# Performance work log

Measured on AMD Instinct MI355X. Metric: run time of the kernel, lower is better.

The kernel has to match this reference:

```python
import jax, jax.numpy as jnp
import numpy as np

# Dims: B batch, C=P channels (features per pixel), H*W=N pixels, M ELM models, Q=1 hidden units
M, Q, B, C, H, W_SP = 4, 1, 32, 1024, 28, 28
P = C
N = H * W_SP
EPS = 1e-10


def _lcg_weights(m, n, seed):
    """Deterministic LCG pseudo-random weights, z-score standardized (ELM_AE init)."""
    L = m * n
    a, b, c = L + 2, L + 3, float(L) ** 2
    v = np.zeros(L, dtype=np.float64)
    v[0] = seed + 1.0
    for i in range(1, L):
        v[i] = (a * v[i - 1] + b) % c
    v = (v - v.mean()) / (v.std() + EPS)
    return v.reshape(m, n).astype(np.float32)


def setup_inputs() -> dict:
    key = jax.random.key(0)
    x = jax.random.normal(key, (B, C, H, W_SP), dtype=jnp.float32)
    # One Q x P random input-weight matrix per ELM model, seed = model * (Q * P)
    Wm = jnp.stack([jnp.asarray(_lcg_weights(Q, P, model * (Q * P))) for model in range(M)])  # [M, Q, P]
    return {"x": x, "Wm": Wm}


def reference(x, Wm):
    b, c, h, w = x.shape
    # _norm('l2', ...): per-channel L2 normalization over (h, w), as F.normalize(dim=(1,2))
    norms = jnp.linalg.norm(x.reshape(b, c, h * w), axis=-1)[:, :, None, None]  # [B, C, 1, 1]
    xn = x / jnp.maximum(norms, EPS)
    X = xn.reshape(b, c, h * w)  # meta activation map per sample: [B, P, N]
    # ELM-AE hidden layer, batched over (sample, model): g = sigmoid(W @ X)
    G = jax.nn.sigmoid(jnp.einsum('mqp,bpn->bmqn', Wm, X))  # [B, M, Q, N]
    # fit_AE: output weights beta = pinv(g^T) @ X^T  -> [Q, P]
    pinvGt = jnp.linalg.pinv(jnp.swapaxes(G, -1, -2))       # [B, M, Q, N]
    beta = jnp.einsum('bmqn,bpn->bmqp', pinvGt, X)          # [B, M, Q, P]
    # sum over the M models; Q == 1 so flatten (Q, P) -> Q*P features
    feats = beta.sum(axis=1).reshape(b, -1)                 # [B, Q*P]
    return jnp.nan_to_num(feats)
```

## Files before the change

### kernel.cpp

```cpp
#include <hip/hip_runtime.h>
#include <math.h>

#define BATCH 32
#define CH    1024
#define NPix  784
#define MMOD  4
#define NPC   16
#define PPC   64
#define T2    832

__device__ __forceinline__ float wave_reduce(float s) {
    #pragma unroll
    for (int off = 32; off; off >>= 1) s += __shfl_down(s, off, 64);
    return s;
}

__global__ __launch_bounds__(T2) void k_norm_z(const float* __restrict__ x,
                                               const float* __restrict__ Wm,
                                               float* __restrict__ inv_norm,
                                               float* __restrict__ zpart) {
    __shared__ float inv_lds[PPC];
    __shared__ float wlds[MMOD][PPC];
    const int blk = blockIdx.x;
    const int b  = blk >> 4;
    const int pc = blk & (NPC - 1);
    const int t = threadIdx.x;
    const int wv = t >> 6, lane = t & 63;
    const float* xb = x + ((size_t)b * CH + (size_t)pc * PPC) * NPix;

    for (int row = wv; row < PPC; row += 13) {
        const float4* r4 = (const float4*)(xb + (size_t)row * NPix);
        float s = 0.f;
        #pragma unroll
        for (int i = 0; i < 3; i++) {
            float4 v = r4[i * 64 + lane];
            s += v.x*v.x + v.y*v.y + v.z*v.z + v.w*v.w;
        }
        if (lane < 4) {
            float4 v = r4[192 + lane];
            s += v.x*v.x + v.y*v.y + v.z*v.z + v.w*v.w;
        }
        s = wave_reduce(s);
        if (lane == 0) {
            float inv = 1.f / fmaxf(sqrtf(s), 1e-10f);
            inv_lds[row] = inv;
            inv_norm[b * CH + pc * PPC + row] = inv;
        }
    }
    __syncthreads();

    if (t < PPC) {
        float inv = inv_lds[t];
        #pragma unroll
        for (int m = 0; m < MMOD; m++)
            wlds[m][t] = Wm[m * CH + pc * PPC + t] * inv;
    }
    __syncthreads();

    if (t < NPix) {
        float a0 = 0.f, a1 = 0.f, a2 = 0.f, a3 = 0.f;
        const float* xp = xb + t;
        #pragma unroll 8
        for (int pp = 0; pp < PPC; pp++) {
            float xv = xp[(size_t)pp * NPix];
            a0 += wlds[0][pp] * xv;
            a1 += wlds[1][pp] * xv;
            a2 += wlds[2][pp] * xv;
            a3 += wlds[3][pp] * xv;
        }
        size_t base = (((size_t)b * NPC + pc) * MMOD) * NPix + t;
        zpart[base]            = a0;
        zpart[base + NPix]     = a1;
        zpart[base + 2 * NPix] = a2;
        zpart[base + 3 * NPix] = a3;
    }
}

__global__ __launch_bounds__(T2) void k_hout(const float* __restrict__ x,
                                             const float* __restrict__ zpart,
                                             const float* __restrict__ inv_norm,
                                             float* __restrict__ out) {
    __shared__ float red[13][MMOD];
    __shared__ float s2s[MMOD];
    __shared__ float h_lds[NPix];
    const int blk = blockIdx.x;
    const int b = blk >> 3;
    const int j = blk & 7;
    const int t = threadIdx.x;
    const int wv = t >> 6, lane = t & 63;
    const bool act = (t < NPix);

    float g[MMOD];
    #pragma unroll
    for (int m = 0; m < MMOD; m++) {
        float z = 0.f;
        if (act) {
            #pragma unroll
            for (int pc = 0; pc < NPC; pc++)
                z += zpart[(((size_t)b * NPC + pc) * MMOD + m) * NPix + t];
        }
        g[m] = act ? 1.f / (1.f + expf(-z)) : 0.f;
    }
    #pragma unroll
    for (int m = 0; m < MMOD; m++) {
        float s = wave_reduce(g[m] * g[m]);
        if (lane == 0) red[wv][m] = s;
    }
    __syncthreads();
    if (t < MMOD) {
        float s = 0.f;
        #pragma unroll
        for (int w = 0; w < 13; w++) s += red[w][t];
        s2s[t] = fmaxf(s, 1e-30f);
    }
    __syncthreads();
    if (act) {
        float hv = 0.f;
        #pragma unroll
        for (int m = 0; m < MMOD; m++) hv += g[m] / s2s[m];
        h_lds[t] = hv;
    }
    __syncthreads();

    const float4* h4 = (const float4*)h_lds;
    for (int rr = wv; rr < 2 * PPC; rr += 13) {
        const int pc = j + 8 * (rr >> 6);
        const int p  = pc * PPC + (rr & 63);
        const int r  = b * CH + p;
        const float4* x4 = (const float4*)(x + (size_t)r * NPix);
        float s = 0.f;
        #pragma unroll
        for (int i = 0; i < 3; i++) {
            float4 xv = x4[i * 64 + lane];
            float4 hv = h4[i * 64 + lane];
            s += xv.x*hv.x + xv.y*hv.y + xv.z*hv.z + xv.w*hv.w;
        }
        if (lane < 4) {
            float4 xv = x4[192 + lane];
            float4 hv = h4[192 + lane];
            s += xv.x*hv.x + xv.y*hv.y + xv.z*hv.z + xv.w*hv.w;
        }
        s = wave_reduce(s);
        if (lane == 0) {
            float v = s * inv_norm[r];
            if (!(v == v)) v = 0.f;
            v = fminf(fmaxf(v, -3.402823466e+38f), 3.402823466e+38f);
            out[r] = v;
        }
    }
}

extern "C" void kernel_launch(void* const* d_in, const int* in_sizes, int n_in,
                              void* d_out, int out_size, void* d_ws, size_t ws_size,
                              hipStream_t stream) {
    const float* x  = (const float*)d_in[0];
    const float* Wm = (const float*)d_in[1];
    float* out = (float*)d_out;
    float* wsf = (float*)d_ws;

    float* inv_norm = wsf;
    float* zpart    = inv_norm + BATCH * CH;

    k_norm_z<<<BATCH * NPC, T2, 0, stream>>>(x, Wm, inv_norm, zpart);
    k_hout<<<BATCH * 8, T2, 0, stream>>>(x, zpart, inv_norm, out);
}
```

Baseline: 186.0 us.

## Fuse norm, projection and output passes into one cooperative kernel with grid syncs

Merges the two kernels into a single cooperative kernel of 256 blocks. Each block owns 128 channels of one sample and computes their norms and partial projections. After a grid sync, one block per sample builds the hidden vector, and after a second sync each block re-reads its own channel slab to form the output. This drops the second launch and the global inverse-norm buffer, and lets the second pass over x hit cache because each block rereads the 400KB it just read. In exchange it adds two grid-wide barriers, and only 256 large blocks do the work, half the first kernel's earlier parallelism.

```diff
diff --git a/kernel.cpp b/kernel.cpp
--- a/kernel.cpp
+++ b/kernel.cpp
@@ -1,13 +1,16 @@
 #include <hip/hip_runtime.h>
+#include <hip/hip_cooperative_groups.h>
 #include <math.h>
+
+namespace cg = cooperative_groups;
 
 #define BATCH 32
 #define CH    1024
 #define NPix  784
 #define MMOD  4
-#define NPC   16
-#define PPC   64
-#define T2    832
+#define JCH   8
+#define CPB   128
+#define TB    832
 
 __device__ __forceinline__ float wave_reduce(float s) {
     #pragma unroll
@@ -15,20 +18,27 @@
     return s;
 }
 
-__global__ __launch_bounds__(T2) void k_norm_z(const float* __restrict__ x,
-                                               const float* __restrict__ Wm,
-                                               float* __restrict__ inv_norm,
-                                               float* __restrict__ zpart) {
-    __shared__ float inv_lds[PPC];
-    __shared__ float wlds[MMOD][PPC];
+__global__ __launch_bounds__(TB) void k_fused(const float* __restrict__ x,
+                                              const float* __restrict__ Wm,
+                                              float* __restrict__ zpart,
+                                              float* __restrict__ h,
+                                              float* __restrict__ out) {
+    __shared__ float inv_l[CPB];
+    __shared__ float wl[MMOD][CPB];
+    __shared__ float h_l[NPix];
+    __shared__ float red[13][MMOD];
+    __shared__ float s2s[MMOD];
+
+    cg::grid_group grid = cg::this_grid();
+
     const int blk = blockIdx.x;
-    const int b  = blk >> 4;
-    const int pc = blk & (NPC - 1);
+    const int b = blk >> 3;
+    const int j = blk & 7;
     const int t = threadIdx.x;
     const int wv = t >> 6, lane = t & 63;
-    const float* xb = x + ((size_t)b * CH + (size_t)pc * PPC) * NPix;
+    const float* xb = x + ((size_t)b * CH + (size_t)j * CPB) * NPix;
 
-    for (int row = wv; row < PPC; row += 13) {
+    for (int row = wv; row < CPB; row += 13) {
         const float4* r4 = (const float4*)(xb + (size_t)row * NPix);
         float s = 0.f;
         #pragma unroll
@@ -41,19 +51,15 @@
             s += v.x*v.x + v.y*v.y + v.z*v.z + v.w*v.w;
         }
         s = wave_reduce(s);
-        if (lane == 0) {
-            float inv = 1.f / fmaxf(sqrtf(s), 1e-10f);
-            inv_lds[row] = inv;
-            inv_norm[b * CH + pc * PPC + row] = inv;
-        }
+        if (lane == 0) inv_l[row] = 1.f / fmaxf(sqrtf(s), 1e-10f);
     }
     __syncthreads();
 
-    if (t < PPC) {
-        float inv = inv_lds[t];
+    if (t < CPB) {
+        float inv = inv_l[t];
         #pragma unroll
         for (int m = 0; m < MMOD; m++)
-            wlds[m][t] = Wm[m * CH + pc * PPC + t] * inv;
+            wl[m][t] = Wm[m * CH + j * CPB + t] * inv;
     }
     __syncthreads();
 
@@ -61,73 +67,63 @@
         float a0 = 0.f, a1 = 0.f, a2 = 0.f, a3 = 0.f;
         const float* xp = xb + t;
         #pragma unroll 8
-        for (int pp = 0; pp < PPC; pp++) {
+        for (int pp = 0; pp < CPB; pp++) {
             float xv = xp[(size_t)pp * NPix];
-            a0 += wlds[0][pp] * xv;
-            a1 += wlds[1][pp] * xv;
-            a2 += wlds[2][pp] * xv;
-            a3 += wlds[3][pp] * xv;
+            a0 += wl[0][pp] * xv;
+            a1 += wl[1][pp] * xv;
+            a2 += wl[2][pp] * xv;
+            a3 += wl[3][pp] * xv;
         }
-        size_t base = (((size_t)b * NPC + pc) * MMOD) * NPix + t;
+        size_t base = ((size_t)blk * MMOD) * NPix + t;
         zpart[base]            = a0;
         zpart[base + NPix]     = a1;
         zpart[base + 2 * NPix] = a2;
         zpart[base + 3 * NPix] = a3;
     }
-}
+    __threadfence();
+    grid.sync();
 
-__global__ __launch_bounds__(T2) void k_hout(const float* __restrict__ x,
-                                             const float* __restrict__ zpart,
-                                             const float* __restrict__ inv_norm,
-                                             float* __restrict__ out) {
-    __shared__ float red[13][MMOD];
-    __shared__ float s2s[MMOD];
-    __shared__ float h_lds[NPix];
-    const int blk = blockIdx.x;
-    const int b = blk >> 3;
-    const int j = blk & 7;
-    const int t = threadIdx.x;
-    const int wv = t >> 6, lane = t & 63;
-    const bool act = (t < NPix);
+    if (j == 0) {
+        const bool act = (t < NPix);
+        float g[MMOD];
+        #pragma unroll
+        for (int m = 0; m < MMOD; m++) {
+            float z = 0.f;
+            if (act) {
+                #pragma unroll
+                for (int jj = 0; jj < JCH; jj++)
+                    z += zpart[(((size_t)(b * JCH + jj)) * MMOD + m) * NPix + t];
+            }
+            g[m] = act ? 1.f / (1.f + expf(-z)) : 0.f;
+        }
+        #pragma unroll
+        for (int m = 0; m < MMOD; m++) {
+            float s = wave_reduce(g[m] * g[m]);
+            if (lane == 0) red[wv][m] = s;
+        }
+        __syncthreads();
+        if (t < MMOD) {
+            float s = 0.f;
+            #pragma unroll
+            for (int w = 0; w < 13; w++) s += red[w][t];
+            s2s[t] = fmaxf(s, 1e-30f);
+        }
+        __syncthreads();
+        if (act) {
+            float hv = 0.f;
+            #pragma unroll
+            for (int m = 0; m < MMOD; m++) hv += g[m] / s2s[m];
+            h[(size_t)b * NPix + t] = hv;
+        }
+    }
+    __threadfence();
+    grid.sync();
 
-    float g[MMOD];
-    #pragma unroll
-    for (int m = 0; m < MMOD; m++) {
-        float z = 0.f;
-        if (act) {
-            #pragma unroll
-            for (int pc = 0; pc < NPC; pc++)
-                z += zpart[(((size_t)b * NPC + pc) * MMOD + m) * NPix + t];
-        }
-        g[m] = act ? 1.f / (1.f + expf(-z)) : 0.f;
-    }
-    #pragma unroll
-    for (int m = 0; m < MMOD; m++) {
-        float s = wave_reduce(g[m] * g[m]);
-        if (lane == 0) red[wv][m] = s;
-    }
+    if (t < NPix) h_l[t] = h[(size_t)b * NPix + t];
     __syncthreads();
-    if (t < MMOD) {
-        float s = 0.f;
-        #pragma unroll
-        for (int w = 0; w < 13; w++) s += red[w][t];
-        s2s[t] = fmaxf(s, 1e-30f);
-    }
-    __syncthreads();
-    if (act) {
-        float hv = 0.f;
-        #pragma unroll
-        for (int m = 0; m < MMOD; m++) hv += g[m] / s2s[m];
-        h_lds[t] = hv;
-    }
-    __syncthreads();
-
-    const float4* h4 = (const float4*)h_lds;
-    for (int rr = wv; rr < 2 * PPC; rr += 13) {
-        const int pc = j + 8 * (rr >> 6);
-        const int p  = pc * PPC + (rr & 63);
-        const int r  = b * CH + p;
-        const float4* x4 = (const float4*)(x + (size_t)r * NPix);
+    const float4* h4 = (const float4*)h_l;
+    for (int row = wv; row < CPB; row += 13) {
+        const float4* x4 = (const float4*)(xb + (size_t)row * NPix);
         float s = 0.f;
         #pragma unroll
         for (int i = 0; i < 3; i++) {
@@ -142,10 +138,10 @@
         }
         s = wave_reduce(s);
         if (lane == 0) {
-            float v = s * inv_norm[r];
+            float v = s * inv_l[row];
             if (!(v == v)) v = 0.f;
             v = fminf(fmaxf(v, -3.402823466e+38f), 3.402823466e+38f);
-            out[r] = v;
+            out[b * CH + j * CPB + row] = v;
         }
     }
 }
@@ -158,9 +154,10 @@
     float* out = (float*)d_out;
     float* wsf = (float*)d_ws;
 
-    float* inv_norm = wsf;
-    float* zpart    = inv_norm + BATCH * CH;
+    float* zpart = wsf;
+    float* h     = zpart + (size_t)BATCH * JCH * MMOD * NPix;
 
-    k_norm_z<<<BATCH * NPC, T2, 0, stream>>>(x, Wm, inv_norm, zpart);
-    k_hout<<<BATCH * 8, T2, 0, stream>>>(x, zpart, inv_norm, out);
+    void* args[] = { (void*)&x, (void*)&Wm, (void*)&zpart, (void*)&h, (void*)&out };
+    hipLaunchCooperativeKernel((const void*)k_fused, dim3(BATCH * JCH), dim3(TB),
+                               args, 0, stream);
 }
```

New measurement: 371.9 us. 100.0% more time.
